# Kernel tuning notes

Measured on AMD Instinct MI355X. Metric: run time of the kernel, lower is better.

## Reference

```python
import jax, jax.numpy as jnp
import numpy as np

B, S, H, D = 32, 2048, 1024, 1024
NEG_BIG = -1e10  # matches torch's -10000000000.0 sentinel


def setup_inputs() -> dict:
    key = jax.random.key(0)
    k1, k2, k3, k4, k5 = jax.random.split(key, 5)
    hidden = jax.random.normal(k1, (B, H), dtype=jnp.float32)
    encoder_outs = jax.random.normal(k2, (B, S, D), dtype=jnp.float32)
    src_lens = jax.random.randint(k3, (B,), 1, S + 1, dtype=jnp.int64 if jax.config.jax_enable_x64 else jnp.int32)
    W1 = jax.random.normal(k4, (D, H), dtype=jnp.float32) * (1.0 / np.sqrt(H))
    W2 = jax.random.normal(k5, (D, H + D), dtype=jnp.float32) * (1.0 / np.sqrt(H + D))
    return {"hidden": hidden, "encoder_outs": encoder_outs, "src_lens": src_lens, "W1": W1, "W2": W2}


def reference(hidden, encoder_outs, src_lens, W1, W2):
    # x = l1(hidden): (B, D)
    x = hidden @ W1.T
    # att_score: (B, S) (torch computes (S, B); we keep batch-major and transpose attn at the end)
    scores = jnp.einsum('bsd,bd->bs', encoder_outs, x)
    seq_len = encoder_outs.shape[1]
    mask = (jnp.arange(seq_len)[None, :] < src_lens[:, None]).astype(scores.dtype)  # (B, S)
    masked = mask * scores
    # torch quirk: exact zeros (masked OR genuinely-zero scores) -> -1e10
    masked = jnp.where(masked == 0.0, jnp.asarray(NEG_BIG, masked.dtype), masked)
    attn = jax.nn.softmax(masked, axis=1)  # softmax over seq dim (torch dim=0 of (S,B))
    ctx = jnp.einsum('bs,bsd->bd', attn, encoder_outs)  # weighted sum: (B, D)
    out = jnp.tanh(jnp.concatenate([ctx, hidden], axis=1) @ W2.T)  # (B, D)
    return out, attn.T  # attn returned as (S, B) to match torch
```

## Files before the change

kernel.cpp:

```cpp
#include <hip/hip_runtime.h>
#include <hip/hip_bf16.h>
#include <math.h>

#define BB 32
#define SS 2048
#define HH 1024
#define DD 1024
#define HD 2048
#define NSPLIT 32
#define KSPLIT 16
#define NEG_BIG -1e10f

__device__ __forceinline__ float wave_reduce_sum(float v) {
#pragma unroll
    for (int off = 32; off > 0; off >>= 1) v += __shfl_xor(v, off, 64);
    return v;
}

__device__ __forceinline__ float dot4(float4 a, float4 b) {
    return a.x * b.x + a.y * b.y + a.z * b.z + a.w * b.w;
}

__global__ __launch_bounds__(256) void k1_gemv_x(const float* __restrict__ hidden,
                                                 const float* __restrict__ W1,
                                                 float* __restrict__ x) {
    __shared__ float4 hs[16 * 256];
    int tid = threadIdx.x;
    int w = tid >> 6, lane = tid & 63;
    int d = blockIdx.x * 4 + w;
    const float4* wp = (const float4*)(W1 + (size_t)d * HH);
    float4 w0 = wp[lane], w1 = wp[lane + 64], w2 = wp[lane + 128], w3 = wp[lane + 192];
    const float4* hp = (const float4*)hidden;

    for (int half = 0; half < 2; ++half) {
        __syncthreads();
#pragma unroll
        for (int i = 0; i < 16; ++i) hs[i * 256 + tid] = hp[half * 4096 + i * 256 + tid];
        __syncthreads();
#pragma unroll
        for (int bl = 0; bl < 16; bl += 2) {
            const float4* hb0 = hs + bl * 256;
            const float4* hb1 = hs + (bl + 1) * 256;
            float s0 = dot4(hb0[lane], w0) + dot4(hb0[lane + 64], w1) +
                       dot4(hb0[lane + 128], w2) + dot4(hb0[lane + 192], w3);
            float s1 = dot4(hb1[lane], w0) + dot4(hb1[lane + 64], w1) +
                       dot4(hb1[lane + 128], w2) + dot4(hb1[lane + 192], w3);
#pragma unroll
            for (int off = 32; off > 0; off >>= 1) {
                s0 += __shfl_xor(s0, off, 64);
                s1 += __shfl_xor(s1, off, 64);
            }
            if (lane == 0) {
                x[(half * 16 + bl) * DD + d] = s0;
                x[(half * 16 + bl + 1) * DD + d] = s1;
            }
        }
    }
}

__global__ __launch_bounds__(512) void k2_fused(const float* __restrict__ enc,
                                                const float* __restrict__ x,
                                                const int* __restrict__ src_lens,
                                                float* __restrict__ scores,
                                                float* __restrict__ ctxp,
                                                float* __restrict__ m_part,
                                                float* __restrict__ l_part) {
    int tid = threadIdx.x;
    int w = tid >> 6, lane = tid & 63;

    __shared__ int pfx[BB + 1];
    if (tid == 0) {
        int a = 0;
        pfx[0] = 0;
#pragma unroll
        for (int b = 0; b < BB; ++b) {
            a += (src_lens[b] + 63) >> 6;
            pfx[b + 1] = a;
        }
    }
    __shared__ float4 lctx[8][256];
    __shared__ float lm[8], ll[8];
    __syncthreads();
    int total = pfx[BB];

    for (int chunk = blockIdx.x; chunk < total; chunk += gridDim.x) {
        int b = 0;
        while (pfx[b + 1] <= chunk) ++b;
        int sp = chunk - pfx[b];
        int len = src_lens[b];
        int srow = sp * 64 + w * 8;

        float m = NEG_BIG, l = 0.f;
        float4 a0 = {0, 0, 0, 0}, a1 = {0, 0, 0, 0}, a2 = {0, 0, 0, 0}, a3 = {0, 0, 0, 0};

        if (srow < len) {
            const float4* xp = (const float4*)(x + (size_t)b * DD);
            float4 x0 = xp[lane], x1 = xp[lane + 64], x2 = xp[lane + 128], x3 = xp[lane + 192];
            int rend = min(8, len - srow);
            const float* erow = enc + ((size_t)b * SS + srow) * DD;
            int r = 0;
            for (; r + 4 <= rend; r += 4) {
                const float4* pr0 = (const float4*)(erow + (size_t)(r + 0) * DD);
                const float4* pr1 = (const float4*)(erow + (size_t)(r + 1) * DD);
                const float4* pr2 = (const float4*)(erow + (size_t)(r + 2) * DD);
                const float4* pr3 = (const float4*)(erow + (size_t)(r + 3) * DD);
                float4 e00 = pr0[lane], e01 = pr0[lane + 64], e02 = pr0[lane + 128], e03 = pr0[lane + 192];
                float4 e10 = pr1[lane], e11 = pr1[lane + 64], e12 = pr1[lane + 128], e13 = pr1[lane + 192];
                float4 e20 = pr2[lane], e21 = pr2[lane + 64], e22 = pr2[lane + 128], e23 = pr2[lane + 192];
                float4 e30 = pr3[lane], e31 = pr3[lane + 64], e32 = pr3[lane + 128], e33 = pr3[lane + 192];
                float p0 = dot4(e00, x0) + dot4(e01, x1) + dot4(e02, x2) + dot4(e03, x3);
                float p1 = dot4(e10, x0) + dot4(e11, x1) + dot4(e12, x2) + dot4(e13, x3);
                float p2 = dot4(e20, x0) + dot4(e21, x1) + dot4(e22, x2) + dot4(e23, x3);
                float p3 = dot4(e30, x0) + dot4(e31, x1) + dot4(e32, x2) + dot4(e33, x3);
#pragma unroll
                for (int off = 32; off > 0; off >>= 1) {
                    p0 += __shfl_xor(p0, off, 64);
                    p1 += __shfl_xor(p1, off, 64);
                    p2 += __shfl_xor(p2, off, 64);
                    p3 += __shfl_xor(p3, off, 64);
                }
                float v0 = (p0 == 0.0f) ? NEG_BIG : p0;
                float v1 = (p1 == 0.0f) ? NEG_BIG : p1;
                float v2 = (p2 == 0.0f) ? NEG_BIG : p2;
                float v3 = (p3 == 0.0f) ? NEG_BIG : p3;
                if (lane == 0) {
                    scores[b * SS + srow + r + 0] = v0;
                    scores[b * SS + srow + r + 1] = v1;
                    scores[b * SS + srow + r + 2] = v2;
                    scores[b * SS + srow + r + 3] = v3;
                }
                float mm = fmaxf(m, fmaxf(fmaxf(v0, v1), fmaxf(v2, v3)));
                float sc = __expf(m - mm);
                m = mm;
                l *= sc;
                a0.x *= sc; a0.y *= sc; a0.z *= sc; a0.w *= sc;
                a1.x *= sc; a1.y *= sc; a1.z *= sc; a1.w *= sc;
                a2.x *= sc; a2.y *= sc; a2.z *= sc; a2.w *= sc;
                a3.x *= sc; a3.y *= sc; a3.z *= sc; a3.w *= sc;
                float q0 = __expf(v0 - mm), q1 = __expf(v1 - mm);
                float q2 = __expf(v2 - mm), q3 = __expf(v3 - mm);
                l += q0 + q1 + q2 + q3;
                a0.x += q0 * e00.x + q1 * e10.x + q2 * e20.x + q3 * e30.x;
                a0.y += q0 * e00.y + q1 * e10.y + q2 * e20.y + q3 * e30.y;
                a0.z += q0 * e00.z + q1 * e10.z + q2 * e20.z + q3 * e30.z;
                a0.w += q0 * e00.w + q1 * e10.w + q2 * e20.w + q3 * e30.w;
                a1.x += q0 * e01.x + q1 * e11.x + q2 * e21.x + q3 * e31.x;
                a1.y += q0 * e01.y + q1 * e11.y + q2 * e21.y + q3 * e31.y;
                a1.z += q0 * e01.z + q1 * e11.z + q2 * e21.z + q3 * e31.z;
                a1.w += q0 * e01.w + q1 * e11.w + q2 * e21.w + q3 * e31.w;
                a2.x += q0 * e02.x + q1 * e12.x + q2 * e22.x + q3 * e32.x;
                a2.y += q0 * e02.y + q1 * e12.y + q2 * e22.y + q3 * e32.y;
                a2.z += q0 * e02.z + q1 * e12.z + q2 * e22.z + q3 * e32.z;
                a2.w += q0 * e02.w + q1 * e12.w + q2 * e22.w + q3 * e32.w;
                a3.x += q0 * e03.x + q1 * e13.x + q2 * e23.x + q3 * e33.x;
                a3.y += q0 * e03.y + q1 * e13.y + q2 * e23.y + q3 * e33.y;
                a3.z += q0 * e03.z + q1 * e13.z + q2 * e23.z + q3 * e33.z;
                a3.w += q0 * e03.w + q1 * e13.w + q2 * e23.w + q3 * e33.w;
            }
            for (; r < rend; ++r) {
                const float4* ep = (const float4*)(erow + (size_t)r * DD);
                float4 e0 = ep[lane], e1 = ep[lane + 64], e2 = ep[lane + 128], e3 = ep[lane + 192];
                float p0 = dot4(e0, x0) + dot4(e1, x1) + dot4(e2, x2) + dot4(e3, x3);
                p0 = wave_reduce_sum(p0);
                float v0 = (p0 == 0.0f) ? NEG_BIG : p0;
                if (lane == 0) scores[b * SS + srow + r] = v0;
                float mm = fmaxf(m, v0);
                float sc = __expf(m - mm);
                m = mm;
                l *= sc;
                a0.x *= sc; a0.y *= sc; a0.z *= sc; a0.w *= sc;
                a1.x *= sc; a1.y *= sc; a1.z *= sc; a1.w *= sc;
                a2.x *= sc; a2.y *= sc; a2.z *= sc; a2.w *= sc;
                a3.x *= sc; a3.y *= sc; a3.z *= sc; a3.w *= sc;
                float q0 = __expf(v0 - mm);
                l += q0;
                a0.x += q0 * e0.x; a0.y += q0 * e0.y; a0.z += q0 * e0.z; a0.w += q0 * e0.w;
                a1.x += q0 * e1.x; a1.y += q0 * e1.y; a1.z += q0 * e1.z; a1.w += q0 * e1.w;
                a2.x += q0 * e2.x; a2.y += q0 * e2.y; a2.z += q0 * e2.z; a2.w += q0 * e2.w;
                a3.x += q0 * e3.x; a3.y += q0 * e3.y; a3.z += q0 * e3.z; a3.w += q0 * e3.w;
            }
        }

        lctx[w][lane] = a0;
        lctx[w][lane + 64] = a1;
        lctx[w][lane + 128] = a2;
        lctx[w][lane + 192] = a3;
        if (lane == 0) { lm[w] = m; ll[w] = l; }
        __syncthreads();

        if (tid < 256) {
            float M = lm[0];
#pragma unroll
            for (int k = 1; k < 8; ++k) M = fmaxf(M, lm[k]);
            float L = 0.f;
            float4 sum = {0, 0, 0, 0};
#pragma unroll
            for (int k = 0; k < 8; ++k) {
                float sc = __expf(lm[k] - M);
                L += sc * ll[k];
                float4 c = lctx[k][tid];
                sum.x += sc * c.x; sum.y += sc * c.y; sum.z += sc * c.z; sum.w += sc * c.w;
            }
            int cc = ((tid >> 6) << 8) | ((tid & 63) << 2);
            *(float4*)(ctxp + ((size_t)(b * NSPLIT + sp)) * DD + cc) = sum;
            if (tid == 0) {
                m_part[b * NSPLIT + sp] = M;
                l_part[b * NSPLIT + sp] = L;
            }
        }
        __syncthreads();
    }
}

__global__ __launch_bounds__(256) void k3_combine(const float* __restrict__ ctxp,
                                                  const float* __restrict__ m_part,
                                                  const float* __restrict__ l_part,
                                                  const int* __restrict__ src_lens,
                                                  float* __restrict__ ctx,
                                                  float* __restrict__ Mb,
                                                  float* __restrict__ Lb) {
    int b = blockIdx.x >> 2;
    int col = (blockIdx.x & 3) * 256 + threadIdx.x;
    int nb = (src_lens[b] + 63) >> 6;
    float M = NEG_BIG;
    for (int k = 0; k < nb; ++k) M = fmaxf(M, m_part[b * NSPLIT + k]);
    float L = 0.f;
    float sum = 0.f;
    for (int k = 0; k < nb; ++k) {
        float sc = __expf(m_part[b * NSPLIT + k] - M);
        L += sc * l_part[b * NSPLIT + k];
        sum += sc * ctxp[((size_t)(b * NSPLIT + k)) * DD + col];
    }
    ctx[(size_t)b * DD + col] = sum / L;
    if (threadIdx.x == 0 && (blockIdx.x & 3) == 0) { Mb[b] = M; Lb[b] = L; }
}

__global__ __launch_bounds__(256) void k5_outgemm(const float* __restrict__ ctx,
                                                  const float* __restrict__ hidden,
                                                  const float* __restrict__ W2,
                                                  float* __restrict__ outp) {
    int dt = blockIdx.x & 31;
    int ks = blockIdx.x >> 5;
    int tid = threadIdx.x;
    __shared__ float cat_s[32 * 128];
    __shared__ float w2_s[32 * 128];
    int b0 = tid & 15, b1 = b0 + 16;
    int dl0 = (tid >> 4) * 2, dl1 = dl0 + 1;
    float acc00 = 0.f, acc01 = 0.f, acc10 = 0.f, acc11 = 0.f;

    int j0 = ks * 128;
#pragma unroll
    for (int pass = 0; pass < 4; ++pass) {
        int r = pass * 8 + (tid >> 5);
        int jj4 = tid & 31;
        int j = j0 + jj4 * 4;
        const float* src = (j < 1024) ? (ctx + (size_t)r * 1024 + j)
                                      : (hidden + (size_t)r * 1024 + (j - 1024));
        float4 v = *(const float4*)src;
        *(float4*)(cat_s + r * 128 + ((jj4 ^ (r & 7)) << 2)) = v;
        int dg = dt * 32 + r;
        float4 wv = *(const float4*)(W2 + (size_t)dg * HD + j);
        *(float4*)(w2_s + r * 128 + ((jj4 ^ (r & 7)) << 2)) = wv;
    }
    __syncthreads();
#pragma unroll 4
    for (int jj4 = 0; jj4 < 32; ++jj4) {
        float4 cA = *(const float4*)(cat_s + b0 * 128 + ((jj4 ^ (b0 & 7)) << 2));
        float4 cB = *(const float4*)(cat_s + b1 * 128 + ((jj4 ^ (b1 & 7)) << 2));
        float4 wA = *(const float4*)(w2_s + dl0 * 128 + ((jj4 ^ (dl0 & 7)) << 2));
        float4 wB = *(const float4*)(w2_s + dl1 * 128 + ((jj4 ^ (dl1 & 7)) << 2));
        acc00 += dot4(cA, wA);
        acc01 += dot4(cA, wB);
        acc10 += dot4(cB, wA);
        acc11 += dot4(cB, wB);
    }
    float* op = outp + (size_t)ks * (BB * DD);
    op[b0 * 1024 + dt * 32 + dl0] = acc00;
    op[b0 * 1024 + dt * 32 + dl1] = acc01;
    op[b1 * 1024 + dt * 32 + dl0] = acc10;
    op[b1 * 1024 + dt * 32 + dl1] = acc11;
}

__global__ __launch_bounds__(256) void k6_final(const float* __restrict__ outp,
                                                const float* __restrict__ scores,
                                                const int* __restrict__ src_lens,
                                                const float* __restrict__ Mb,
                                                const float* __restrict__ Lb,
                                                float* __restrict__ out) {
    int i = blockIdx.x * 256 + threadIdx.x;
    if (i < BB * DD) {
        float s = 0.f;
#pragma unroll
        for (int k = 0; k < KSPLIT; ++k) s += outp[(size_t)k * (BB * DD) + i];
        out[i] = tanhf(s);
    } else {
        int j = i - BB * DD;
        int b = j & 31, sIdx = j >> 5;
        float v = 0.0f;
        if (sIdx < src_lens[b]) v = __expf(scores[b * SS + sIdx] - Mb[b]) / Lb[b];
        out[i] = v;
    }
}

extern "C" void kernel_launch(void* const* d_in, const int* in_sizes, int n_in,
                              void* d_out, int out_size, void* d_ws, size_t ws_size,
                              hipStream_t stream) {
    const float* hidden = (const float*)d_in[0];
    const float* enc = (const float*)d_in[1];
    const int* src_lens = (const int*)d_in[2];
    const float* W1 = (const float*)d_in[3];
    const float* W2 = (const float*)d_in[4];
    float* out = (float*)d_out;
    float* ws = (float*)d_ws;

    float* x = ws;
    float* scores = ws + 32768;
    float* ctxp = ws + 98304;
    float* m_part = ws + 1146880;
    float* l_part = ws + 1147904;
    float* Mb = ws + 1148928;
    float* Lb = ws + 1148960;
    float* ctx = ws + 1148992;
    float* outp = ws + 1181760;

    k1_gemv_x<<<256, 256, 0, stream>>>(hidden, W1, x);
    k2_fused<<<512, 512, 0, stream>>>(enc, x, src_lens, scores, ctxp, m_part, l_part);
    k3_combine<<<128, 256, 0, stream>>>(ctxp, m_part, l_part, src_lens, ctx, Mb, Lb);
    k5_outgemm<<<512, 256, 0, stream>>>(ctx, hidden, W2, outp);
    k6_final<<<384, 256, 0, stream>>>(outp, scores, src_lens, Mb, Lb, out);
}
```

Before: 57.54 us.

## Fuse output GEMM with final tanh/attn kernel, removing split-K partials

Combines the split-K output GEMM and the final reduction/attention-normalisation kernel into one launch. GEMM blocks now loop over the full K dimension for 16 output columns each and apply tanh directly, which removes the partial-sum workspace round trip and one kernel launch. The cost is that the GEMM runs on only 64 blocks with a serial K loop, which reduces parallelism for streaming W2.

```diff
diff --git a/kernel.cpp b/kernel.cpp
--- a/kernel.cpp
+++ b/kernel.cpp
@@ -8,7 +8,6 @@
 #define DD 1024
 #define HD 2048
 #define NSPLIT 32
-#define KSPLIT 16
 #define NEG_BIG -1e10f
 
 __device__ __forceinline__ float wave_reduce_sum(float v) {
@@ -235,70 +234,63 @@
     if (threadIdx.x == 0 && (blockIdx.x & 3) == 0) { Mb[b] = M; Lb[b] = L; }
 }
 
-__global__ __launch_bounds__(256) void k5_outgemm(const float* __restrict__ ctx,
-                                                  const float* __restrict__ hidden,
-                                                  const float* __restrict__ W2,
-                                                  float* __restrict__ outp) {
-    int dt = blockIdx.x & 31;
-    int ks = blockIdx.x >> 5;
+__global__ __launch_bounds__(256) void k45_out(const float* __restrict__ ctx,
+                                               const float* __restrict__ hidden,
+                                               const float* __restrict__ W2,
+                                               const float* __restrict__ scores,
+                                               const int* __restrict__ src_lens,
+                                               const float* __restrict__ Mb,
+                                               const float* __restrict__ Lb,
+                                               float* __restrict__ out) {
+    int blk = blockIdx.x;
     int tid = threadIdx.x;
-    __shared__ float cat_s[32 * 128];
-    __shared__ float w2_s[32 * 128];
-    int b0 = tid & 15, b1 = b0 + 16;
-    int dl0 = (tid >> 4) * 2, dl1 = dl0 + 1;
-    float acc00 = 0.f, acc01 = 0.f, acc10 = 0.f, acc11 = 0.f;
-
-    int j0 = ks * 128;
-#pragma unroll
-    for (int pass = 0; pass < 4; ++pass) {
-        int r = pass * 8 + (tid >> 5);
-        int jj4 = tid & 31;
-        int j = j0 + jj4 * 4;
-        const float* src = (j < 1024) ? (ctx + (size_t)r * 1024 + j)
-                                      : (hidden + (size_t)r * 1024 + (j - 1024));
-        float4 v = *(const float4*)src;
-        *(float4*)(cat_s + r * 128 + ((jj4 ^ (r & 7)) << 2)) = v;
-        int dg = dt * 32 + r;
-        float4 wv = *(const float4*)(W2 + (size_t)dg * HD + j);
-        *(float4*)(w2_s + r * 128 + ((jj4 ^ (r & 7)) << 2)) = wv;
-    }
-    __syncthreads();
+    if (blk < 64) {
+        int dt = blk;
+        __shared__ float cat_s[32 * 128];
+        __shared__ float w2_s[16 * 128];
+        int b0 = tid & 15, b1 = b0 + 16;
+        int dl = tid >> 4;
+        float acc0 = 0.f, acc1 = 0.f;
+
+        for (int ks = 0; ks < 16; ++ks) {
+            int j0 = ks * 128;
+            __syncthreads();
+#pragma unroll
+            for (int pass = 0; pass < 4; ++pass) {
+                int r = pass * 8 + (tid >> 5);
+                int jj4 = tid & 31;
+                int j = j0 + jj4 * 4;
+                const float* src = (j < 1024) ? (ctx + (size_t)r * 1024 + j)
+                                              : (hidden + (size_t)r * 1024 + (j - 1024));
+                float4 v = *(const float4*)src;
+                *(float4*)(cat_s + r * 128 + ((jj4 ^ (r & 7)) << 2)) = v;
+            }
+#pragma unroll
+            for (int pass = 0; pass < 2; ++pass) {
+                int r = pass * 8 + (tid >> 5);
+                int jj4 = tid & 31;
+                int j = j0 + jj4 * 4;
+                float4 wv = *(const float4*)(W2 + (size_t)(dt * 16 + r) * HD + j);
+                *(float4*)(w2_s + r * 128 + ((jj4 ^ (r & 7)) << 2)) = wv;
+            }
+            __syncthreads();
 #pragma unroll 4
-    for (int jj4 = 0; jj4 < 32; ++jj4) {
-        float4 cA = *(const float4*)(cat_s + b0 * 128 + ((jj4 ^ (b0 & 7)) << 2));
-        float4 cB = *(const float4*)(cat_s + b1 * 128 + ((jj4 ^ (b1 & 7)) << 2));
-        float4 wA = *(const float4*)(w2_s + dl0 * 128 + ((jj4 ^ (dl0 & 7)) << 2));
-        float4 wB = *(const float4*)(w2_s + dl1 * 128 + ((jj4 ^ (dl1 & 7)) << 2));
-        acc00 += dot4(cA, wA);
-        acc01 += dot4(cA, wB);
-        acc10 += dot4(cB, wA);
-        acc11 += dot4(cB, wB);
-    }
-    float* op = outp + (size_t)ks * (BB * DD);
-    op[b0 * 1024 + dt * 32 + dl0] = acc00;
-    op[b0 * 1024 + dt * 32 + dl1] = acc01;
-    op[b1 * 1024 + dt * 32 + dl0] = acc10;
-    op[b1 * 1024 + dt * 32 + dl1] = acc11;
-}
-
-__global__ __launch_bounds__(256) void k6_final(const float* __restrict__ outp,
-                                                const float* __restrict__ scores,
-                                                const int* __restrict__ src_lens,
-                                                const float* __restrict__ Mb,
-                                                const float* __restrict__ Lb,
-                                                float* __restrict__ out) {
-    int i = blockIdx.x * 256 + threadIdx.x;
-    if (i < BB * DD) {
-        float s = 0.f;
-#pragma unroll
-        for (int k = 0; k < KSPLIT; ++k) s += outp[(size_t)k * (BB * DD) + i];
-        out[i] = tanhf(s);
+            for (int jj4 = 0; jj4 < 32; ++jj4) {
+                float4 cA = *(const float4*)(cat_s + b0 * 128 + ((jj4 ^ (b0 & 7)) << 2));
+                float4 cB = *(const float4*)(cat_s + b1 * 128 + ((jj4 ^ (b1 & 7)) << 2));
+                float4 wA = *(const float4*)(w2_s + dl * 128 + ((jj4 ^ (dl & 7)) << 2));
+                acc0 += dot4(cA, wA);
+                acc1 += dot4(cB, wA);
+            }
+        }
+        out[b0 * 1024 + dt * 16 + dl] = tanhf(acc0);
+        out[b1 * 1024 + dt * 16 + dl] = tanhf(acc1);
     } else {
-        int j = i - BB * DD;
+        int j = (blk - 64) * 256 + tid;
         int b = j & 31, sIdx = j >> 5;
         float v = 0.0f;
         if (sIdx < src_lens[b]) v = __expf(scores[b * SS + sIdx] - Mb[b]) / Lb[b];
-        out[i] = v;
+        out[BB * DD + j] = v;
     }
 }
 
@@ -321,11 +313,9 @@
     float* Mb = ws + 1148928;
     float* Lb = ws + 1148960;
     float* ctx = ws + 1148992;
-    float* outp = ws + 1181760;
 
     k1_gemv_x<<<256, 256, 0, stream>>>(hidden, W1, x);
     k2_fused<<<512, 512, 0, stream>>>(enc, x, src_lens, scores, ctxp, m_part, l_part);
     k3_combine<<<128, 256, 0, stream>>>(ctxp, m_part, l_part, src_lens, ctx, Mb, Lb);
-    k5_outgemm<<<512, 256, 0, stream>>>(ctx, hidden, W2, outp);
-    k6_final<<<384, 256, 0, stream>>>(outp, scores, src_lens, Mb, Lb, out);
-}
+    k45_out<<<320, 256, 0, stream>>>(ctx, hidden, W2, scores, src_lens, Mb, Lb, out);
+}
```

Result: slower. 94.07 us (+63.5%).
